# Kernel tuning notes

Hardware: AMD Instinct MI355X
Metric: run time of the kernel (lower is better)

The kernel has to match this reference:

```python
import jax, jax.numpy as jnp
import numpy as np

N = 8192  # n_nodes
E = 262144  # edges per adjacency (avg degree 32)


def setup_inputs() -> dict:
    key = jax.random.key(0)
    k0, k1, k2, k3, k4, k5 = jax.random.split(key, 6)
    rows_s = jax.random.randint(k0, (E,), 0, N)
    cols_s = jax.random.randint(k1, (E,), 0, N)
    vals_s = jax.random.uniform(k2, (E,), dtype=jnp.float32)
    rows_t = jax.random.randint(k3, (E,), 0, N)
    cols_t = jax.random.randint(k4, (E,), 0, N)
    vals_t = jax.random.uniform(k5, (E,), dtype=jnp.float32)
    gamma = jnp.zeros((1,), dtype=jnp.float32)  # learnable scalar, init 0.0
    return {
        "rows_s": rows_s, "cols_s": cols_s, "vals_s": vals_s,
        "rows_t": rows_t, "cols_t": cols_t, "vals_t": vals_t,
        "gamma": gamma,
    }


def reference(rows_s, cols_s, vals_s, rows_t, cols_t, vals_t, gamma):
    # coalesce + to_dense: scatter-add duplicates into dense [N, N]
    As = jnp.zeros((N, N), dtype=vals_s.dtype).at[rows_s, cols_s].add(vals_s)
    At = jnp.zeros((N, N), dtype=vals_t.dtype).at[rows_t, cols_t].add(vals_t)
    alpha = jax.nn.sigmoid(gamma[0])
    Af = alpha * As + (1.0 - alpha) * At
    row_sum = jnp.sum(Af, axis=1, keepdims=True)  # [N, 1]
    row_sum = jnp.where(row_sum == 0, jnp.ones_like(row_sum), row_sum)
    Af = Af / row_sum
    # torch returns Af.to_sparse(); dense Af is the equivalent value-complete output
    return Af
```

## Files before the change

### kernel.cpp

```cpp
#include <hip/hip_runtime.h>
#include <math.h>

#define NN 8192
#define NE 262144
#define TOTAL (2*NE)
#define CAP 128

typedef float f4 __attribute__((ext_vector_type(4)));

struct Pair { int c; float v; };

#define BK_OFF (65536)
#define OV_OFF (65536 + (size_t)NN * CAP * 8)

__global__ __launch_bounds__(256) void fill_kernel(
        const int* __restrict__ rows_s, const int* __restrict__ cols_s,
        const float* __restrict__ vals_s,
        const int* __restrict__ rows_t, const int* __restrict__ cols_t,
        const float* __restrict__ vals_t,
        const float* __restrict__ gamma,
        int* __restrict__ cnt, Pair* __restrict__ bucket,
        int* __restrict__ ovf_cnt, int4* __restrict__ ovf) {
    int i = blockIdx.x * blockDim.x + threadIdx.x;
    float alpha = 1.0f / (1.0f + expf(-gamma[0]));
    int r, c; float v, w;
    if (i < NE) { r = rows_s[i]; c = cols_s[i]; v = vals_s[i]; w = alpha; }
    else { int j = i - NE; r = rows_t[j]; c = cols_t[j]; v = vals_t[j]; w = 1.0f - alpha; }
    float wv = w * v;
    int pos = atomicAdd(&cnt[r], 1);
    if (pos < CAP) {
        Pair p; p.c = c; p.v = wv;
        bucket[r * CAP + pos] = p;
    } else {
        int k = atomicAdd(ovf_cnt, 1);
        int4 e; e.x = r; e.y = c; e.z = __float_as_int(wv); e.w = 0;
        ovf[k] = e;
    }
}

__global__ __launch_bounds__(256) void row_kernel(
        const int* __restrict__ cnt, const Pair* __restrict__ bucket,
        const int* __restrict__ ovf_cnt, const int4* __restrict__ ovf,
        float* __restrict__ out) {
    __shared__ float row[NN];
    __shared__ float red[4];
    int r = blockIdx.x;
    int t = threadIdx.x;

    f4* row4 = (f4*)row;
    #pragma unroll
    for (int k = t; k < NN / 4; k += 256) {
        f4 z = {0.f, 0.f, 0.f, 0.f};
        row4[k] = z;
    }
    int n = cnt[r];
    int nb = n < CAP ? n : CAP;
    __syncthreads();

    float part = 0.0f;
    for (int k = t; k < nb; k += 256) {
        Pair p = bucket[r * CAP + k];
        part += p.v;
        atomicAdd(&row[p.c], p.v);
    }
    int no = *ovf_cnt;
    if (no > 0) {
        for (int k = t; k < no; k += 256) {
            int4 e = ovf[k];
            if (e.x == r) {
                float v = __int_as_float(e.z);
                part += v;
                atomicAdd(&row[e.y], v);
            }
        }
    }

    #pragma unroll
    for (int o = 32; o > 0; o >>= 1) part += __shfl_down(part, o, 64);
    if ((t & 63) == 0) red[t >> 6] = part;
    __syncthreads();
    float total = red[0] + red[1] + red[2] + red[3];
    float inv = (total == 0.0f) ? 1.0f : 1.0f / total;

    f4* out4 = (f4*)(out + (size_t)r * NN);
    #pragma unroll
    for (int k = t; k < NN / 4; k += 256) {
        f4 x = row4[k];
        x *= inv;
        __builtin_nontemporal_store(x, &out4[k]);
    }
}

extern "C" void kernel_launch(void* const* d_in, const int* in_sizes, int n_in,
                              void* d_out, int out_size, void* d_ws, size_t ws_size,
                              hipStream_t stream) {
    const int*   rows_s = (const int*)  d_in[0];
    const int*   cols_s = (const int*)  d_in[1];
    const float* vals_s = (const float*)d_in[2];
    const int*   rows_t = (const int*)  d_in[3];
    const int*   cols_t = (const int*)  d_in[4];
    const float* vals_t = (const float*)d_in[5];
    const float* gamma  = (const float*)d_in[6];

    float* out     = (float*)d_out;
    char*  ws      = (char*)d_ws;
    int*   cnt     = (int*)ws;
    int*   ovf_cnt = (int*)(ws + 32768);
    Pair*  bucket  = (Pair*)(ws + BK_OFF);
    int4*  ovf     = (int4*)(ws + OV_OFF);

    (void)hipMemsetAsync(ws, 0, 32772, stream);

    fill_kernel<<<TOTAL / 256, 256, 0, stream>>>(rows_s, cols_s, vals_s,
                                                 rows_t, cols_t, vals_t,
                                                 gamma, cnt, bucket, ovf_cnt, ovf);
    row_kernel<<<NN, 256, 0, stream>>>(cnt, bucket, ovf_cnt, ovf, out);
}
```

Before: 311.5 us.

## Split each output row across two blocks and pad per-row counters

```diff
diff --git a/kernel.cpp b/kernel.cpp
--- a/kernel.cpp
+++ b/kernel.cpp
@@ -5,13 +5,16 @@
 #define NE 262144
 #define TOTAL (2*NE)
 #define CAP 128
+#define CSTR 16
+#define HALF 4096
 
 typedef float f4 __attribute__((ext_vector_type(4)));
 
 struct Pair { int c; float v; };
 
-#define BK_OFF (65536)
-#define OV_OFF (65536 + (size_t)NN * CAP * 8)
+#define CNT_BYTES ((size_t)NN * CSTR * 4)
+#define BK_OFF ((size_t)1 << 20)
+#define OV_OFF (BK_OFF + (size_t)NN * CAP * sizeof(Pair))
 
 __global__ __launch_bounds__(256) void fill_kernel(
         const int* __restrict__ rows_s, const int* __restrict__ cols_s,
@@ -27,7 +30,7 @@
     if (i < NE) { r = rows_s[i]; c = cols_s[i]; v = vals_s[i]; w = alpha; }
     else { int j = i - NE; r = rows_t[j]; c = cols_t[j]; v = vals_t[j]; w = 1.0f - alpha; }
     float wv = w * v;
-    int pos = atomicAdd(&cnt[r], 1);
+    int pos = atomicAdd(&cnt[r * CSTR], 1);
     if (pos < CAP) {
         Pair p; p.c = c; p.v = wv;
         bucket[r * CAP + pos] = p;
@@ -42,18 +45,20 @@
         const int* __restrict__ cnt, const Pair* __restrict__ bucket,
         const int* __restrict__ ovf_cnt, const int4* __restrict__ ovf,
         float* __restrict__ out) {
-    __shared__ float row[NN];
+    __shared__ float row[HALF];
     __shared__ float red[4];
-    int r = blockIdx.x;
+    int b = blockIdx.x;
+    int r = b >> 1;
+    int base = (b & 1) << 12;
     int t = threadIdx.x;
 
     f4* row4 = (f4*)row;
     #pragma unroll
-    for (int k = t; k < NN / 4; k += 256) {
+    for (int k = t; k < HALF / 4; k += 256) {
         f4 z = {0.f, 0.f, 0.f, 0.f};
         row4[k] = z;
     }
-    int n = cnt[r];
+    int n = cnt[r * CSTR];
     int nb = n < CAP ? n : CAP;
     __syncthreads();
 
@@ -61,7 +66,8 @@
     for (int k = t; k < nb; k += 256) {
         Pair p = bucket[r * CAP + k];
         part += p.v;
-        atomicAdd(&row[p.c], p.v);
+        int cl = p.c - base;
+        if ((unsigned)cl < HALF) atomicAdd(&row[cl], p.v);
     }
     int no = *ovf_cnt;
     if (no > 0) {
@@ -70,7 +76,8 @@
             if (e.x == r) {
                 float v = __int_as_float(e.z);
                 part += v;
-                atomicAdd(&row[e.y], v);
+                int cl = e.y - base;
+                if ((unsigned)cl < HALF) atomicAdd(&row[cl], v);
             }
         }
     }
@@ -82,9 +89,9 @@
     float total = red[0] + red[1] + red[2] + red[3];
     float inv = (total == 0.0f) ? 1.0f : 1.0f / total;
 
-    f4* out4 = (f4*)(out + (size_t)r * NN);
+    f4* out4 = (f4*)(out + (size_t)r * NN + base);
     #pragma unroll
-    for (int k = t; k < NN / 4; k += 256) {
+    for (int k = t; k < HALF / 4; k += 256) {
         f4 x = row4[k];
         x *= inv;
         __builtin_nontemporal_store(x, &out4[k]);
@@ -105,14 +112,14 @@
     float* out     = (float*)d_out;
     char*  ws      = (char*)d_ws;
     int*   cnt     = (int*)ws;
-    int*   ovf_cnt = (int*)(ws + 32768);
+    int*   ovf_cnt = (int*)(ws + CNT_BYTES);
     Pair*  bucket  = (Pair*)(ws + BK_OFF);
     int4*  ovf     = (int4*)(ws + OV_OFF);
 
-    (void)hipMemsetAsync(ws, 0, 32772, stream);
+    (void)hipMemsetAsync(ws, 0, CNT_BYTES + 4, stream);
 
     fill_kernel<<<TOTAL / 256, 256, 0, stream>>>(rows_s, cols_s, vals_s,
                                                  rows_t, cols_t, vals_t,
                                                  gamma, cnt, bucket, ovf_cnt, ovf);
-    row_kernel<<<NN, 256, 0, stream>>>(cnt, bucket, ovf_cnt, ovf, out);
+    row_kernel<<<2 * NN, 256, 0, stream>>>(cnt, bucket, ovf_cnt, ovf, out);
 }
```

After: 313.7 us. Within noise of the previous version (+0.7%).

## Replace row-bucket pipeline with rowsum pass and direct global atomic scatter

Applied to the files above, without the earlier changes.

```diff
diff --git a/kernel.cpp b/kernel.cpp
--- a/kernel.cpp
+++ b/kernel.cpp
@@ -4,91 +4,49 @@
 #define NN 8192
 #define NE 262144
 #define TOTAL (2*NE)
-#define CAP 128
+#define CSTR 16
+#define CNT_BYTES ((size_t)NN * CSTR * 4)
 
 typedef float f4 __attribute__((ext_vector_type(4)));
 
-struct Pair { int c; float v; };
+#define NF4 (NN * (size_t)NN / 4)
 
-#define BK_OFF (65536)
-#define OV_OFF (65536 + (size_t)NN * CAP * 8)
+__global__ __launch_bounds__(256) void zero_rowsum_kernel(
+        const int* __restrict__ rows_s, const float* __restrict__ vals_s,
+        const int* __restrict__ rows_t, const float* __restrict__ vals_t,
+        const float* __restrict__ gamma,
+        float* __restrict__ rowsum, float* __restrict__ out) {
+    int i = blockIdx.x * blockDim.x + threadIdx.x;
+    float alpha = 1.0f / (1.0f + expf(-gamma[0]));
+    int r; float wv;
+    if (i < NE) { r = rows_s[i]; wv = alpha * vals_s[i]; }
+    else { int j = i - NE; r = rows_t[j]; wv = (1.0f - alpha) * vals_t[j]; }
+    atomicAdd(&rowsum[r * CSTR], wv);
 
-__global__ __launch_bounds__(256) void fill_kernel(
+    f4* out4 = (f4*)out;
+    f4 z = {0.f, 0.f, 0.f, 0.f};
+    #pragma unroll
+    for (int k = 0; k < 32; ++k) {
+        __builtin_nontemporal_store(z, &out4[(size_t)k * TOTAL + i]);
+    }
+}
+
+__global__ __launch_bounds__(256) void scatter_kernel(
         const int* __restrict__ rows_s, const int* __restrict__ cols_s,
         const float* __restrict__ vals_s,
         const int* __restrict__ rows_t, const int* __restrict__ cols_t,
         const float* __restrict__ vals_t,
         const float* __restrict__ gamma,
-        int* __restrict__ cnt, Pair* __restrict__ bucket,
-        int* __restrict__ ovf_cnt, int4* __restrict__ ovf) {
+        const float* __restrict__ rowsum,
+        float* __restrict__ out) {
     int i = blockIdx.x * blockDim.x + threadIdx.x;
     float alpha = 1.0f / (1.0f + expf(-gamma[0]));
-    int r, c; float v, w;
-    if (i < NE) { r = rows_s[i]; c = cols_s[i]; v = vals_s[i]; w = alpha; }
-    else { int j = i - NE; r = rows_t[j]; c = cols_t[j]; v = vals_t[j]; w = 1.0f - alpha; }
-    float wv = w * v;
-    int pos = atomicAdd(&cnt[r], 1);
-    if (pos < CAP) {
-        Pair p; p.c = c; p.v = wv;
-        bucket[r * CAP + pos] = p;
-    } else {
-        int k = atomicAdd(ovf_cnt, 1);
-        int4 e; e.x = r; e.y = c; e.z = __float_as_int(wv); e.w = 0;
-        ovf[k] = e;
-    }
-}
-
-__global__ __launch_bounds__(256) void row_kernel(
-        const int* __restrict__ cnt, const Pair* __restrict__ bucket,
-        const int* __restrict__ ovf_cnt, const int4* __restrict__ ovf,
-        float* __restrict__ out) {
-    __shared__ float row[NN];
-    __shared__ float red[4];
-    int r = blockIdx.x;
-    int t = threadIdx.x;
-
-    f4* row4 = (f4*)row;
-    #pragma unroll
-    for (int k = t; k < NN / 4; k += 256) {
-        f4 z = {0.f, 0.f, 0.f, 0.f};
-        row4[k] = z;
-    }
-    int n = cnt[r];
-    int nb = n < CAP ? n : CAP;
-    __syncthreads();
-
-    float part = 0.0f;
-    for (int k = t; k < nb; k += 256) {
-        Pair p = bucket[r * CAP + k];
-        part += p.v;
-        atomicAdd(&row[p.c], p.v);
-    }
-    int no = *ovf_cnt;
-    if (no > 0) {
-        for (int k = t; k < no; k += 256) {
-            int4 e = ovf[k];
-            if (e.x == r) {
-                float v = __int_as_float(e.z);
-                part += v;
-                atomicAdd(&row[e.y], v);
-            }
-        }
-    }
-
-    #pragma unroll
-    for (int o = 32; o > 0; o >>= 1) part += __shfl_down(part, o, 64);
-    if ((t & 63) == 0) red[t >> 6] = part;
-    __syncthreads();
-    float total = red[0] + red[1] + red[2] + red[3];
-    float inv = (total == 0.0f) ? 1.0f : 1.0f / total;
-
-    f4* out4 = (f4*)(out + (size_t)r * NN);
-    #pragma unroll
-    for (int k = t; k < NN / 4; k += 256) {
-        f4 x = row4[k];
-        x *= inv;
-        __builtin_nontemporal_store(x, &out4[k]);
-    }
+    int r, c; float wv;
+    if (i < NE) { r = rows_s[i]; c = cols_s[i]; wv = alpha * vals_s[i]; }
+    else { int j = i - NE; r = rows_t[j]; c = cols_t[j]; wv = (1.0f - alpha) * vals_t[j]; }
+    float s = rowsum[r * CSTR];
+    float q = wv / (s == 0.0f ? 1.0f : s);
+    atomicAdd(&out[(size_t)r * NN + c], q);
 }
 
 extern "C" void kernel_launch(void* const* d_in, const int* in_sizes, int n_in,
@@ -102,17 +60,13 @@
     const float* vals_t = (const float*)d_in[5];
     const float* gamma  = (const float*)d_in[6];
 
-    float* out     = (float*)d_out;
-    char*  ws      = (char*)d_ws;
-    int*   cnt     = (int*)ws;
-    int*   ovf_cnt = (int*)(ws + 32768);
-    Pair*  bucket  = (Pair*)(ws + BK_OFF);
-    int4*  ovf     = (int4*)(ws + OV_OFF);
+    float* out    = (float*)d_out;
+    float* rowsum = (float*)d_ws;
 
-    (void)hipMemsetAsync(ws, 0, 32772, stream);
+    (void)hipMemsetAsync(d_ws, 0, CNT_BYTES, stream);
 
-    fill_kernel<<<TOTAL / 256, 256, 0, stream>>>(rows_s, cols_s, vals_s,
-                                                 rows_t, cols_t, vals_t,
-                                                 gamma, cnt, bucket, ovf_cnt, ovf);
-    row_kernel<<<NN, 256, 0, stream>>>(cnt, bucket, ovf_cnt, ovf, out);
+    zero_rowsum_kernel<<<TOTAL / 256, 256, 0, stream>>>(
+        rows_s, vals_s, rows_t, vals_t, gamma, rowsum, out);
+    scatter_kernel<<<TOTAL / 256, 256, 0, stream>>>(
+        rows_s, cols_s, vals_s, rows_t, cols_t, vals_t, gamma, rowsum, out);
 }
```

Measured after the change: 380.2 us. 1.22x slower.
